# Kernel optimization log

Hardware: AMD Instinct MI355X
Metric: run time of the kernel (lower is better)

Reference implementation:

```python
import jax, jax.numpy as jnp
import numpy as np

H = 128          # hidden/context/decoder dim
HEADS = 4
HEAD_DIM = H // HEADS
MAX_LENGTH = 64
VOCAB = 3


def _lstm_step(h, c, x, Wih, Whh, b):
    # PyTorch gate order: i, f, g, o
    gates = x @ Wih.T + h @ Whh.T + b
    i, f, g, o = jnp.split(gates, 4, axis=-1)
    c = jax.nn.sigmoid(f) * c + jax.nn.sigmoid(i) * jnp.tanh(g)
    h = jax.nn.sigmoid(o) * jnp.tanh(c)
    return h, c


def _run_lstm(x, Wih, Whh, b):
    # x: (T, B, D) -> (T, B, H); zero initial state (PyTorch default)
    B = x.shape[1]
    Hh = Whh.shape[1]
    init = (jnp.zeros((B, Hh), x.dtype), jnp.zeros((B, Hh), x.dtype))
    def step(carry, xt):
        h, c = carry
        h, c = _lstm_step(h, c, xt, Wih, Whh, b)
        return (h, c), h
    _, ys = jax.lax.scan(step, init, x)
    return ys


def setup_inputs() -> dict:
    key = jax.random.key(0)
    T, B, D = 512, 64, 1024
    ks = jax.random.split(key, 20)
    def p(k, shape, s=0.05):
        return jax.random.normal(k, shape, dtype=jnp.float32) * s
    return {
        "cnn_output": p(ks[0], (T, B, D), 1.0),
        # encoder LSTM (2 layers); biases fused (b_ih + b_hh)
        "enc_Wih0": p(ks[1], (4 * H, D)),
        "enc_Whh0": p(ks[2], (4 * H, H)),
        "enc_b0": p(ks[3], (4 * H,)),
        "enc_Wih1": p(ks[4], (4 * H, H)),
        "enc_Whh1": p(ks[5], (4 * H, H)),
        "enc_b1": p(ks[6], (4 * H,)),
        # MultiheadAttention(embed_dim=128, num_heads=4)
        "attn_in_w": p(ks[7], (3 * H, H)),
        "attn_in_b": p(ks[8], (3 * H,)),
        "attn_out_w": p(ks[9], (H, H)),
        "attn_out_b": p(ks[10], (H,)),
        # decoder LSTM (2 layers), input dim 256
        "dec_Wih0": p(ks[11], (4 * H, 2 * H)),
        "dec_Whh0": p(ks[12], (4 * H, H)),
        "dec_b0": p(ks[13], (4 * H,)),
        "dec_Wih1": p(ks[14], (4 * H, H)),
        "dec_Whh1": p(ks[15], (4 * H, H)),
        "dec_b1": p(ks[16], (4 * H,)),
        # output projection
        "lin_w": p(ks[17], (VOCAB, H)),
        "lin_b": p(ks[18], (VOCAB,)),
    }


def reference(cnn_output, enc_Wih0, enc_Whh0, enc_b0, enc_Wih1, enc_Whh1, enc_b1,
              attn_in_w, attn_in_b, attn_out_w, attn_out_b,
              dec_Wih0, dec_Whh0, dec_b0, dec_Wih1, dec_Whh1, dec_b1,
              lin_w, lin_b):
    T, B, _ = cnn_output.shape
    # ---- encoder: 2-layer LSTM over T ----
    enc = _run_lstm(cnn_output, enc_Wih0, enc_Whh0, enc_b0)
    enc = _run_lstm(enc, enc_Wih1, enc_Whh1, enc_b1)          # (T, B, H)

    # ---- precompute attention keys/values (encoding is fixed) ----
    Wq, Wk, Wv = jnp.split(attn_in_w, 3, axis=0)
    bq, bk, bv = jnp.split(attn_in_b, 3, axis=0)
    K = (enc @ Wk.T + bk).reshape(T, B, HEADS, HEAD_DIM)      # (T,B,h,d)
    V = (enc @ Wv.T + bv).reshape(T, B, HEADS, HEAD_DIM)
    scale = 1.0 / np.sqrt(HEAD_DIM)

    # ---- 64-step attention + 2-layer LSTM decode loop ----
    out0 = jnp.zeros((B, H), cnn_output.dtype)
    h0 = jnp.zeros((2, B, H), cnn_output.dtype)
    c0 = jnp.zeros((2, B, H), cnn_output.dtype)

    def step(carry, _):
        out, h, c = carry
        q = ((out @ Wq.T + bq) * scale).reshape(B, HEADS, HEAD_DIM)
        scores = jnp.einsum("bhd,tbhd->bht", q, K)            # (B,h,T)
        attn = jax.nn.softmax(scores, axis=-1)
        ctx = jnp.einsum("bht,tbhd->bhd", attn, V).reshape(B, H)
        ctx = ctx @ attn_out_w.T + attn_out_b
        x = jnp.concatenate([out, ctx], axis=-1)              # (B, 2H)
        nh0, nc0 = _lstm_step(h[0], c[0], x, dec_Wih0, dec_Whh0, dec_b0)
        nh1, nc1 = _lstm_step(h[1], c[1], nh0, dec_Wih1, dec_Whh1, dec_b1)
        new_out = jax.nn.relu(nh1)
        y = new_out @ lin_w.T + lin_b                          # (B, vocab)
        return (new_out, jnp.stack([nh0, nh1]), jnp.stack([nc0, nc1])), y

    _, ys = jax.lax.scan(step, (out0, h0, c0), None, length=MAX_LENGTH)
    return ys                                                  # (64, B, vocab)
```

## Files before the change

kernel.cpp:

```cpp
#include <hip/hip_runtime.h>
#include <math.h>

#define T_LEN 512
#define BATCH 64
#define HID 128
#define G4 512

#define OFF_WQ2   0
#define OFF_WXO   16384
#define OFF_WXC   81920
#define OFF_WHH0b 147456
#define OFF_WIH1b 212992
#define OFF_WHH1b 278528
#define W2_TOTAL  344064

typedef __attribute__((ext_vector_type(8))) short short8b;
typedef __attribute__((ext_vector_type(4))) float f32x4;

__device__ __forceinline__ float sigf(float x) { return 1.0f / (1.0f + __expf(-x)); }
__device__ __forceinline__ float tanhfast(float x) {
    float e = __expf(2.f * x);
    return 1.f - 2.f / (e + 1.f);
}

__device__ __forceinline__ unsigned short f2bf(float x) {
    unsigned u = __float_as_uint(x);
    unsigned r = (u + 0x7fffu + ((u >> 16) & 1u)) >> 16;
    return (unsigned short)r;
}
__device__ __forceinline__ float bf2f(unsigned short u) {
    return __uint_as_float((unsigned)u << 16);
}

__device__ __forceinline__ void cvt8(uint4 u, float f[8]) {
    f[0] = __uint_as_float(u.x << 16); f[1] = __uint_as_float(u.x & 0xffff0000u);
    f[2] = __uint_as_float(u.y << 16); f[3] = __uint_as_float(u.y & 0xffff0000u);
    f[4] = __uint_as_float(u.z << 16); f[5] = __uint_as_float(u.z & 0xffff0000u);
    f[6] = __uint_as_float(u.w << 16); f[7] = __uint_as_float(u.w & 0xffff0000u);
}

#define KEEP4(Vv) asm volatile("" : "+v"((Vv).x), "+v"((Vv).y), "+v"((Vv).z), "+v"((Vv).w))

__device__ __forceinline__ void cstore(float* p, float v) {
    __hip_atomic_store(p, v, __ATOMIC_RELAXED, __HIP_MEMORY_SCOPE_AGENT);
}
__device__ __forceinline__ float cload(float* p) {
    return __hip_atomic_load(p, __ATOMIC_RELAXED, __HIP_MEMORY_SCOPE_AGENT);
}

__global__ __launch_bounds__(256) void pack_bf(
    const float* __restrict__ src, unsigned short* __restrict__ dst, long n8)
{
    long i = (long)blockIdx.x * 256 + threadIdx.x;
    long stride = (long)gridDim.x * 256;
    for (; i < n8; i += stride) {
        const float* s = src + i * 8;
        float4 a = *(const float4*)s;
        float4 b = *(const float4*)(s + 4);
        uint4 o;
        o.x = (unsigned)f2bf(a.x) | ((unsigned)f2bf(a.y) << 16);
        o.y = (unsigned)f2bf(a.z) | ((unsigned)f2bf(a.w) << 16);
        o.z = (unsigned)f2bf(b.x) | ((unsigned)f2bf(b.y) << 16);
        o.w = (unsigned)f2bf(b.z) | ((unsigned)f2bf(b.w) << 16);
        *(uint4*)(dst + i * 8) = o;
    }
}

__global__ __launch_bounds__(256) void gemm_mfma_bf16(
    const unsigned short* __restrict__ A, const unsigned short* __restrict__ B,
    const float* __restrict__ bias, unsigned short* __restrict__ C,
    int M, int N, int K)
{
    __shared__ __align__(16) unsigned char As[128 * 128];
    __shared__ __align__(16) unsigned char Bs[128 * 128];
    const int tid = threadIdx.x;
    const int lane = tid & 63, wave = tid >> 6;
    const int wr = wave >> 1, wc = wave & 1;
    const int m0 = blockIdx.y * 128, n0 = blockIdx.x * 128;
    f32x4 acc[4][4] = {};
    const int lr = lane & 15, g = lane >> 4;

    for (int k0 = 0; k0 < K; k0 += 64) {
        __syncthreads();
        #pragma unroll
        for (int i = 0; i < 4; ++i) {
            int c = tid + i * 256;
            int row = c >> 3, cb = (c & 7) * 16;
            int swz = cb ^ ((row & 7) << 4);
            uint4 va = *(const uint4*)(A + (size_t)(m0 + row) * K + k0 + (c & 7) * 8);
            *(uint4*)(As + row * 128 + swz) = va;
            uint4 vb = *(const uint4*)(B + (size_t)(n0 + row) * K + k0 + (c & 7) * 8);
            *(uint4*)(Bs + row * 128 + swz) = vb;
        }
        __syncthreads();
        #pragma unroll
        for (int kh = 0; kh < 2; ++kh) {
            const int cb = kh * 64 + g * 16;
            short8b af[4], bfr[4];
            #pragma unroll
            for (int m = 0; m < 4; ++m) {
                int row = wr * 64 + m * 16 + lr;
                af[m] = *(const short8b*)(As + row * 128 + (cb ^ ((row & 7) << 4)));
            }
            #pragma unroll
            for (int n = 0; n < 4; ++n) {
                int row = wc * 64 + n * 16 + lr;
                bfr[n] = *(const short8b*)(Bs + row * 128 + (cb ^ ((row & 7) << 4)));
            }
            #pragma unroll
            for (int m = 0; m < 4; ++m)
                #pragma unroll
                for (int n = 0; n < 4; ++n)
                    acc[m][n] = __builtin_amdgcn_mfma_f32_16x16x32_bf16(
                        af[m], bfr[n], acc[m][n], 0, 0, 0);
        }
    }
    #pragma unroll
    for (int n = 0; n < 4; ++n) {
        int col = n0 + wc * 64 + n * 16 + lr;
        float bv = bias[col];
        #pragma unroll
        for (int m = 0; m < 4; ++m) {
            #pragma unroll
            for (int j = 0; j < 4; ++j) {
                int row = m0 + wr * 64 + m * 16 + g * 4 + j;
                C[(size_t)row * N + col] = f2bf(acc[m][n][j] + bv);
            }
        }
    }
}

__global__ __launch_bounds__(1024) void lstm_rec3(
    const unsigned short* __restrict__ X,
    const float* __restrict__ Whh,
    unsigned short* __restrict__ HoutB)
{
    const int b = blockIdx.x;
    const int tid = threadIdx.x;
    const int r = tid >> 1, half = tid & 1;
    __shared__ __align__(16) float h_s[HID];
    __shared__ float gate_s[G4];
    float4 w4[16];
    {
        const float4* wr4 = (const float4*)(Whh + (size_t)r * HID + half * 64);
        #pragma unroll
        for (int i = 0; i < 16; ++i) w4[i] = wr4[i];
    }
    float c = 0.f;
    if (tid < HID) h_s[tid] = 0.f;
    __syncthreads();
    float xc0 = 0.f, xc1 = 0.f, xc2 = 0.f, xc3 = 0.f;
    if (half == 0) {
        xc0 = bf2f(X[(size_t)(0 * BATCH + b) * G4 + r]);
        xc1 = bf2f(X[(size_t)(1 * BATCH + b) * G4 + r]);
        xc2 = bf2f(X[(size_t)(2 * BATCH + b) * G4 + r]);
        xc3 = bf2f(X[(size_t)(3 * BATCH + b) * G4 + r]);
    }
    for (int tc = 0; tc < T_LEN; tc += 4) {
        float xn0 = 0.f, xn1 = 0.f, xn2 = 0.f, xn3 = 0.f;
        if (half == 0 && tc + 4 < T_LEN) {
            xn0 = bf2f(X[(size_t)((tc + 4) * BATCH + b) * G4 + r]);
            xn1 = bf2f(X[(size_t)((tc + 5) * BATCH + b) * G4 + r]);
            xn2 = bf2f(X[(size_t)((tc + 6) * BATCH + b) * G4 + r]);
            xn3 = bf2f(X[(size_t)((tc + 7) * BATCH + b) * G4 + r]);
        }
        #pragma unroll
        for (int i = 0; i < 4; ++i) {
            const int t = tc + i;
            const float xv = (i == 0) ? xc0 : (i == 1) ? xc1 : (i == 2) ? xc2 : xc3;
            float a0 = 0.f, a1 = 0.f, a2 = 0.f, a3 = 0.f;
            const float4* h4 = (const float4*)(h_s + half * 64);
            #pragma unroll
            for (int k = 0; k < 16; ++k) {
                float4 hv = h4[k];
                a0 = fmaf(w4[k].x, hv.x, a0);
                a1 = fmaf(w4[k].y, hv.y, a1);
                a2 = fmaf(w4[k].z, hv.z, a2);
                a3 = fmaf(w4[k].w, hv.w, a3);
            }
            float tot = (a0 + a1) + (a2 + a3);
            tot += __shfl_xor(tot, 1);
            if (half == 0) gate_s[r] = tot + xv;
            __syncthreads();
            if (tid < HID) {
                float gi = gate_s[tid], gf = gate_s[HID+tid], gg = gate_s[2*HID+tid], go = gate_s[3*HID+tid];
                c = sigf(gf) * c + sigf(gi) * tanhfast(gg);
                float h = sigf(go) * tanhfast(c);
                h_s[tid] = h;
                HoutB[(size_t)(t * BATCH + b) * HID + tid] = f2bf(h);
            }
            __syncthreads();
        }
        xc0 = xn0; xc1 = xn1; xc2 = xn2; xc3 = xn3;
    }
}

__global__ __launch_bounds__(256) void kv_pack_bf(
    const unsigned short* __restrict__ KVbf, unsigned short* __restrict__ Kb,
    unsigned short* __restrict__ Vt)
{
    const int b = blockIdx.x & 63, tc = blockIdx.x >> 6;
    const int t0 = tc * 128;
    __shared__ unsigned short tile[128][130];
    const int half = threadIdx.x >> 7;
    const int d = threadIdx.x & 127;
    for (int tt = 0; tt < 128; tt += 2) {
        int trow = tt + half;
        int t = t0 + trow;
        const unsigned short* src = KVbf + ((size_t)t * BATCH + b) * 256;
        Kb[((size_t)b * T_LEN + t) * HID + d] = src[d];
        tile[trow][d] = src[128 + d];
    }
    __syncthreads();
    for (int dd = 0; dd < 128; dd += 2) {
        int drow = dd + half;
        int ts = threadIdx.x & 127;
        Vt[((size_t)b * HID + drow) * T_LEN + t0 + ts] = tile[ts][drow];
    }
}

__global__ __launch_bounds__(256) void pack2(
    const float* __restrict__ attn_in_w,
    const float* __restrict__ dWih0, const float* __restrict__ dWhh0,
    const float* __restrict__ dWih1, const float* __restrict__ dWhh1,
    unsigned short* __restrict__ Wb2)
{
    int i = blockIdx.x * 256 + threadIdx.x;
    if (i >= W2_TOTAL) return;
    if (i >= OFF_WXC && i < OFF_WHH0b) return;
    float v;
    if (i < OFF_WXO) v = attn_in_w[i];
    else if (i < OFF_WXC) {
        int j = i - OFF_WXO; v = dWih0[(size_t)(j >> 7) * 256 + (j & 127)];
    }
    else if (i < OFF_WIH1b) v = dWhh0[i - OFF_WHH0b];
    else if (i < OFF_WHH1b) v = dWih1[i - OFF_WIH1b];
    else                    v = dWhh1[i - OFF_WHH1b];
    Wb2[i] = f2bf(v);
}

__global__ __launch_bounds__(256) void fuse_wxc(
    const float* __restrict__ dWih0, const float* __restrict__ ow,
    unsigned short* __restrict__ Wb2)
{
    __shared__ float ow_s[128 * 128];
    for (int i = threadIdx.x; i < 16384; i += 256) ow_s[i] = ow[i];
    __syncthreads();
    const int r = blockIdx.x * 2 + (threadIdx.x >> 7);
    const int c = threadIdx.x & 127;
    const float* wr = dWih0 + (size_t)r * 256 + 128;
    float acc = 0.f;
    #pragma unroll 8
    for (int j = 0; j < 128; ++j) acc = fmaf(wr[j], ow_s[j * 128 + c], acc);
    Wb2[OFF_WXC + r * 128 + c] = f2bf(acc);
}

__global__ __launch_bounds__(128) void fuse_b0(
    const float* __restrict__ dWih0, const float* __restrict__ ob,
    const float* __restrict__ db0, float* __restrict__ b0p)
{
    int r = blockIdx.x * 128 + threadIdx.x;
    const float* wr = dWih0 + (size_t)r * 256 + 128;
    float acc = db0[r];
    #pragma unroll 8
    for (int j = 0; j < 128; ++j) acc = fmaf(wr[j], ob[j], acc);
    b0p[r] = acc;
}

__global__ __launch_bounds__(512, 2) void decoder7(
    const unsigned short* __restrict__ Kb, const unsigned short* __restrict__ Vt,
    const unsigned short* __restrict__ Wb2, const float* __restrict__ b0p,
    const float* __restrict__ attn_b, const float* __restrict__ b1,
    const float* __restrict__ lw, const float* __restrict__ lb,
    int* __restrict__ flags, float* __restrict__ exh0, float* __restrict__ exh1,
    float* __restrict__ Y)
{
    extern __shared__ __align__(16) char dyn[];
    char* Kl = dyn;
    const int wid = blockIdx.x;
    const int b = wid & 63;
    const int half64 = wid >> 6;
    const int dbase = half64 * 64;
    const int pbase = 64 - dbase;
    const int tid = threadIdx.x;
    int* myflag = flags + wid * 16;
    int* pflag  = flags + (wid ^ 64) * 16;
    float* exh0b = exh0 + b * 256;
    float* exh1b = exh1 + b * 256;

    __shared__ __align__(16) float x_s[384];
    __shared__ __align__(16) float x1_s[256];
    __shared__ __align__(16) float q_s[HID];
    __shared__ __align__(16) float sc[4 * T_LEN];
    __shared__ float red[512];
    __shared__ __align__(16) float ctxp[4][HID];
    __shared__ float g_s[256];
    __shared__ float hmax[4], hden[4];

    {
        const unsigned short* Ksrc = Kb + (size_t)b * T_LEN * HID;
        for (int c = tid; c < T_LEN * HID / 8; c += 512) {
            int t = c >> 4, k16 = c & 15;
            uint4 v = *(const uint4*)(Ksrc + c * 8);
            *(uint4*)(Kl + t * 256 + ((k16 * 16) ^ ((t & 15) << 4))) = v;
        }
    }
    const int lr = tid >> 1, halfk = tid & 1;
    const int r0 = (lr >> 6) * 128 + dbase + (lr & 63);
    uint4 W0[24], W1[16], WQ[4];
    #pragma unroll
    for (int i = 0; i < 24; ++i) {
        int ge = halfk * 192 + i * 8;
        const unsigned short* src =
            (ge < 128) ? Wb2 + OFF_WXO   + (size_t)r0 * HID + ge
          : (ge < 256) ? Wb2 + OFF_WXC   + (size_t)r0 * HID + (ge - 128)
                       : Wb2 + OFF_WHH0b + (size_t)r0 * HID + (ge - 256);
        W0[i] = *(const uint4*)src;
    }
    #pragma unroll
    for (int i = 0; i < 16; ++i) {
        int ge = halfk * 128 + i * 8;
        const unsigned short* src =
            (ge < 128) ? Wb2 + OFF_WIH1b + (size_t)r0 * HID + ge
                       : Wb2 + OFF_WHH1b + (size_t)r0 * HID + (ge - 128);
        W1[i] = *(const uint4*)src;
    }
    const int qrow = tid >> 2, qpart = tid & 3;
    #pragma unroll
    for (int i = 0; i < 4; ++i)
        WQ[i] = *(const uint4*)(Wb2 + OFF_WQ2 + (size_t)qrow * HID + qpart * 32 + i * 8);
    #pragma unroll
    for (int i = 0; i < 24; ++i) KEEP4(W0[i]);
    #pragma unroll
    for (int i = 0; i < 16; ++i) KEEP4(W1[i]);
    #pragma unroll
    for (int i = 0; i < 4; ++i) KEEP4(WQ[i]);

    const float b0r = b0p[r0];
    const float b1r = b1[r0];
    const float bqv = attn_b[qrow];
    float c0 = 0.f, c1 = 0.f;
    if (tid < 384) x_s[tid] = 0.f;
    if (tid < 256) x1_s[tid] = 0.f;
    __syncthreads();
    const float scale = 0.17677669529663687f;
    const int g = tid >> 7, l = tid & 127;

    for (int step = 0; step < 64; ++step) {
        #pragma unroll
        for (int i = 0; i < 24; ++i) KEEP4(W0[i]);
        #pragma unroll
        for (int i = 0; i < 16; ++i) KEEP4(W1[i]);
        #pragma unroll
        for (int i = 0; i < 4; ++i) KEEP4(WQ[i]);
        const int par = step & 1;
        if (step > 0) {
            if (tid == 0)
                while (__hip_atomic_load(pflag, __ATOMIC_RELAXED, __HIP_MEMORY_SCOPE_AGENT) < 2*step + 1)
                    __builtin_amdgcn_s_sleep(1);
            asm volatile("" ::: "memory");
            __syncthreads();
            if (tid < 64) {
                float hp = cload(&exh1b[((step - 1) & 1) * 128 + pbase + tid]);
                x1_s[128 + pbase + tid] = hp;
                x_s[pbase + tid] = fmaxf(hp, 0.f);
            }
            __syncthreads();
        }
        if (step > 0 && half64 == 0 && tid < 24) {
            const int row = tid >> 3, part = tid & 7;
            const float* wr = lw + row * HID + part * 16;
            const float* os = x_s + part * 16;
            float acc = 0.f;
            #pragma unroll
            for (int k = 0; k < 16; ++k) acc = fmaf(wr[k], os[k], acc);
            acc += __shfl_xor(acc, 1);
            acc += __shfl_xor(acc, 2);
            acc += __shfl_xor(acc, 4);
            if (part == 0) Y[((size_t)(step - 1) * BATCH + b) * 3 + row] = acc + lb[row];
        }
        {
            float acc = 0.f;
            const float* os = x_s + qpart * 32;
            #pragma unroll
            for (int i = 0; i < 4; ++i) {
                float f[8]; cvt8(WQ[i], f);
                const float* o8 = os + i * 8;
                acc += f[0]*o8[0]+f[1]*o8[1]+f[2]*o8[2]+f[3]*o8[3]
                     + f[4]*o8[4]+f[5]*o8[5]+f[6]*o8[6]+f[7]*o8[7];
            }
            acc += __shfl_xor(acc, 1);
            acc += __shfl_xor(acc, 2);
            if (qpart == 0) q_s[qrow] = (acc + bqv) * scale;
        }
        __syncthreads();
        {
            const int t = tid;
            float acc[4] = {0.f, 0.f, 0.f, 0.f};
            #pragma unroll
            for (int k16 = 0; k16 < 16; ++k16) {
                uint4 u = *(const uint4*)(Kl + t * 256 + ((k16 * 16) ^ ((t & 15) << 4)));
                float f[8]; cvt8(u, f);
                float4 q0 = *(const float4*)(q_s + k16 * 8);
                float4 q1 = *(const float4*)(q_s + k16 * 8 + 4);
                acc[k16 >> 2] += f[0]*q0.x + f[1]*q0.y + f[2]*q0.z + f[3]*q0.w
                               + f[4]*q1.x + f[5]*q1.y + f[6]*q1.z + f[7]*q1.w;
            }
            #pragma unroll
            for (int h = 0; h < 4; ++h) sc[h * T_LEN + t] = acc[h];
        }
        __syncthreads();
        float v[4];
        float mx = -3.4e38f;
        #pragma unroll
        for (int i = 0; i < 4; ++i) { v[i] = sc[g*T_LEN + l + 128*i]; mx = fmaxf(mx, v[i]); }
        red[tid] = mx;
        __syncthreads();
        if (l < 64) {
            float m2 = fmaxf(red[g*128 + l], red[g*128 + l + 64]);
            #pragma unroll
            for (int s = 32; s > 0; s >>= 1) m2 = fmaxf(m2, __shfl_xor(m2, s, 64));
            if (l == 0) hmax[g] = m2;
        }
        __syncthreads();
        float hm = hmax[g];
        float s4 = 0.f;
        #pragma unroll
        for (int i = 0; i < 4; ++i) {
            float e = __expf(v[i] - hm);
            sc[g*T_LEN + l + 128*i] = e;
            s4 += e;
        }
        red[tid] = s4;
        __syncthreads();
        if (l < 64) {
            float s2 = red[g*128 + l] + red[g*128 + l + 64];
            #pragma unroll
            for (int s = 32; s > 0; s >>= 1) s2 += __shfl_xor(s2, s, 64);
            if (l == 0) hden[g] = s2;
        }
        __syncthreads();
        {
            const int d = tid & 127, ch = tid >> 7;
            const unsigned short* vr = Vt + ((size_t)b * HID + d) * T_LEN + ch * 128;
            const float* scr = sc + (d >> 5) * T_LEN + ch * 128;
            float acc = 0.f;
            #pragma unroll
            for (int k = 0; k < 128; k += 8) {
                float f[8]; cvt8(*(const uint4*)(vr + k), f);
                #pragma unroll
                for (int j = 0; j < 8; ++j) acc = fmaf(f[j], scr[k + j], acc);
            }
            ctxp[ch][d] = acc;
        }
        __syncthreads();
        if (tid < HID)
            x_s[HID + tid] = (ctxp[0][tid] + ctxp[1][tid] + ctxp[2][tid] + ctxp[3][tid]) / hden[tid >> 5];
        __syncthreads();
        {
            float acc = 0.f;
            #pragma unroll
            for (int i = 0; i < 24; ++i) {
                float f[8]; cvt8(W0[i], f);
                const float* xp = x_s + halfk * 192 + i * 8;
                acc += f[0]*xp[0]+f[1]*xp[1]+f[2]*xp[2]+f[3]*xp[3]
                     + f[4]*xp[4]+f[5]*xp[5]+f[6]*xp[6]+f[7]*xp[7];
            }
            acc += __shfl_xor(acc, 1);
            if (halfk == 0) g_s[lr] = acc + b0r;
        }
        __syncthreads();
        if (tid < 64) {
            float gi = g_s[tid], gf = g_s[64+tid], gg = g_s[128+tid], go = g_s[192+tid];
            c0 = sigf(gf) * c0 + sigf(gi) * tanhf(gg);
            float h = sigf(go) * tanhf(c0);
            x_s[256 + dbase + tid] = h;
            x1_s[dbase + tid] = h;
            cstore(&exh0b[par * 128 + dbase + tid], h);
        }
        __syncthreads();
        if (tid == 0) {
            asm volatile("s_waitcnt vmcnt(0)" ::: "memory");
            __hip_atomic_store(myflag, 2*step + 2, __ATOMIC_RELEASE, __HIP_MEMORY_SCOPE_AGENT);
        }
        if (tid == 0)
            while (__hip_atomic_load(pflag, __ATOMIC_ACQUIRE, __HIP_MEMORY_SCOPE_AGENT) < 2*step + 2)
                __builtin_amdgcn_s_sleep(1);
        asm volatile("" ::: "memory");
        __syncthreads();
        if (tid < 64) {
            float hp = cload(&exh0b[par * 128 + pbase + tid]);
            x_s[256 + pbase + tid] = hp;
            x1_s[pbase + tid] = hp;
        }
        __syncthreads();
        {
            float acc = 0.f;
            #pragma unroll
            for (int i = 0; i < 16; ++i) {
                float f[8]; cvt8(W1[i], f);
                const float* xp = x1_s + halfk * 128 + i * 8;
                acc += f[0]*xp[0]+f[1]*xp[1]+f[2]*xp[2]+f[3]*xp[3]
                     + f[4]*xp[4]+f[5]*xp[5]+f[6]*xp[6]+f[7]*xp[7];
            }
            acc += __shfl_xor(acc, 1);
            if (halfk == 0) g_s[lr] = acc + b1r;
        }
        __syncthreads();
        if (tid < 64) {
            float gi = g_s[tid], gf = g_s[64+tid], gg = g_s[128+tid], go = g_s[192+tid];
            c1 = sigf(gf) * c1 + sigf(gi) * tanhf(gg);
            float h = sigf(go) * tanhf(c1);
            x1_s[128 + dbase + tid] = h;
            x_s[dbase + tid] = fmaxf(h, 0.f);
            cstore(&exh1b[par * 128 + dbase + tid], h);
        }
        __syncthreads();
        if (tid == 0) {
            asm volatile("s_waitcnt vmcnt(0)" ::: "memory");
            __hip_atomic_store(myflag, 2*step + 3, __ATOMIC_RELEASE, __HIP_MEMORY_SCOPE_AGENT);
        }
        __syncthreads();
    }
    if (tid == 0)
        while (__hip_atomic_load(pflag, __ATOMIC_ACQUIRE, __HIP_MEMORY_SCOPE_AGENT) < 129)
            __builtin_amdgcn_s_sleep(1);
    asm volatile("" ::: "memory");
    __syncthreads();
    if (tid < 64)
        x_s[pbase + tid] = fmaxf(cload(&exh1b[128 + pbase + tid]), 0.f);
    __syncthreads();
    if (half64 == 0 && tid < 24) {
        const int row = tid >> 3, part = tid & 7;
        const float* wr = lw + row * HID + part * 16;
        const float* os = x_s + part * 16;
        float acc = 0.f;
        #pragma unroll
        for (int k = 0; k < 16; ++k) acc = fmaf(wr[k], os[k], acc);
        acc += __shfl_xor(acc, 1);
        acc += __shfl_xor(acc, 2);
        acc += __shfl_xor(acc, 4);
        if (part == 0) Y[((size_t)63 * BATCH + b) * 3 + row] = acc + lb[row];
    }
}

extern "C" void kernel_launch(void* const* d_in, const int* in_sizes, int n_in,
                              void* d_out, int out_size, void* d_ws, size_t ws_size,
                              hipStream_t stream) {
    const float* cnn        = (const float*)d_in[0];
    const float* eWih0      = (const float*)d_in[1];
    const float* eWhh0      = (const float*)d_in[2];
    const float* eb0        = (const float*)d_in[3];
    const float* eWih1      = (const float*)d_in[4];
    const float* eWhh1      = (const float*)d_in[5];
    const float* eb1        = (const float*)d_in[6];
    const float* attn_in_w  = (const float*)d_in[7];
    const float* attn_in_b  = (const float*)d_in[8];
    const float* attn_out_w = (const float*)d_in[9];
    const float* attn_out_b = (const float*)d_in[10];
    const float* dWih0      = (const float*)d_in[11];
    const float* dWhh0      = (const float*)d_in[12];
    const float* db0        = (const float*)d_in[13];
    const float* dWih1      = (const float*)d_in[14];
    const float* dWhh1      = (const float*)d_in[15];
    const float* db1        = (const float*)d_in[16];
    const float* lin_w      = (const float*)d_in[17];
    const float* lin_b      = (const float*)d_in[18];
    float* Y  = (float*)d_out;

    const int M = T_LEN * BATCH;

    char* wsb = (char*)d_ws;
    unsigned short* Xbf   = (unsigned short*)(wsb);
    unsigned short* Hbf   = (unsigned short*)(wsb + ((size_t)32 << 20));
    unsigned short* wih0b = (unsigned short*)(wsb + ((size_t)40 << 20));
    unsigned short* wih1b = (unsigned short*)(wsb + ((size_t)41 << 20));
    unsigned short* wkvb  = (unsigned short*)(wsb + ((size_t)41 << 20) + (512 << 10));
    unsigned short* Wb2   = (unsigned short*)(wsb + ((size_t)42 << 20));
    float* b0p   = (float*)(wsb + ((size_t)43 << 20));
    int*   flags = (int*)((char*)b0p + 4096);
    float* exh0  = (float*)((char*)flags + 16384);
    float* exh1  = exh0 + 64 * 256;
    unsigned short* cnn_bf = (unsigned short*)(wsb + ((size_t)44 << 20));
    unsigned short* KVbf   = cnn_bf;
    unsigned short* Kb     = (unsigned short*)(wsb + ((size_t)60 << 20));
    unsigned short* Vt     = (unsigned short*)(wsb + ((size_t)68 << 20));

    (void)hipFuncSetAttribute((const void*)decoder7,
                              hipFuncAttributeMaxDynamicSharedMemorySize, 131072);

    pack_bf<<<2048, 256, 0, stream>>>(cnn, cnn_bf, (long)M * 1024 / 8);
    pack_bf<<<256, 256, 0, stream>>>(eWih0, wih0b, (long)512 * 1024 / 8);
    pack_bf<<<32, 256, 0, stream>>>(eWih1, wih1b, (long)512 * 128 / 8);
    pack_bf<<<16, 256, 0, stream>>>(attn_in_w + 128 * 128, wkvb, (long)256 * 128 / 8);
    gemm_mfma_bf16<<<dim3(4, M/128), 256, 0, stream>>>(cnn_bf, wih0b, eb0, Xbf, M, 512, 1024);
    (void)hipMemsetAsync(flags, 0, 16384 + 2 * 64 * 256 * 4, stream);
    pack2<<<(W2_TOTAL + 255) / 256, 256, 0, stream>>>(attn_in_w, dWih0, dWhh0, dWih1, dWhh1, Wb2);
    fuse_wxc<<<256, 256, 0, stream>>>(dWih0, attn_out_w, Wb2);
    fuse_b0<<<4, 128, 0, stream>>>(dWih0, attn_out_b, db0, b0p);
    lstm_rec3<<<BATCH, 1024, 0, stream>>>(Xbf, eWhh0, Hbf);
    gemm_mfma_bf16<<<dim3(4, M/128), 256, 0, stream>>>(Hbf, wih1b, eb1, Xbf, M, 512, 128);
    lstm_rec3<<<BATCH, 1024, 0, stream>>>(Xbf, eWhh1, Hbf);
    gemm_mfma_bf16<<<dim3(2, M/128), 256, 0, stream>>>(Hbf, wkvb, attn_in_b + 128, KVbf, M, 256, 128);
    kv_pack_bf<<<256, 256, 0, stream>>>(KVbf, Kb, Vt);
    decoder7<<<128, 512, 131072, stream>>>(Kb, Vt, Wb2, b0p,
                                           attn_in_b, db1, lin_w, lin_b,
                                           flags, exh0, exh1, Y);
}
```

Before: 2.468 ms.

## Shuffle-exchange LSTM gates, double-buffer hidden state, drop softmax max pass

The encoder LSTM recurrence remaps threads so that the four gate rows of one hidden unit sit in the same wavefront. Gates are exchanged with lane shuffles instead of shared memory, and the hidden state is double-buffered, which removes one block barrier per timestep. The decoder drops the softmax max-subtraction pass, exponentiating raw scores directly, and reduces the context partial sums with shuffles instead of a shared-memory round trip. Skipping the max subtraction removes two barriers and a reduction, but it risks overflow if attention scores grow large.

```diff
diff --git a/kernel.cpp b/kernel.cpp
--- a/kernel.cpp
+++ b/kernel.cpp
@@ -130,16 +130,20 @@
     }
 }
 
-__global__ __launch_bounds__(1024) void lstm_rec3(
+__global__ __launch_bounds__(1024) void lstm_rec4(
     const unsigned short* __restrict__ X,
     const float* __restrict__ Whh,
     unsigned short* __restrict__ HoutB)
 {
     const int b = blockIdx.x;
     const int tid = threadIdx.x;
-    const int r = tid >> 1, half = tid & 1;
-    __shared__ __align__(16) float h_s[HID];
-    __shared__ float gate_s[G4];
+    const int j = tid >> 3;
+    const int gg = (tid >> 1) & 3;
+    const int half = tid & 1;
+    const int r = gg * 128 + j;
+    const int lane = tid & 63;
+    const int base = lane & ~7;
+    __shared__ __align__(16) float h_s[2][HID];
     float4 w4[16];
     {
         const float4* wr4 = (const float4*)(Whh + (size_t)r * HID + half * 64);
@@ -147,7 +151,7 @@
         for (int i = 0; i < 16; ++i) w4[i] = wr4[i];
     }
     float c = 0.f;
-    if (tid < HID) h_s[tid] = 0.f;
+    if (tid < HID) h_s[0][tid] = 0.f;
     __syncthreads();
     float xc0 = 0.f, xc1 = 0.f, xc2 = 0.f, xc3 = 0.f;
     if (half == 0) {
@@ -167,9 +171,10 @@
         #pragma unroll
         for (int i = 0; i < 4; ++i) {
             const int t = tc + i;
+            const int rb = t & 1, wb = rb ^ 1;
             const float xv = (i == 0) ? xc0 : (i == 1) ? xc1 : (i == 2) ? xc2 : xc3;
             float a0 = 0.f, a1 = 0.f, a2 = 0.f, a3 = 0.f;
-            const float4* h4 = (const float4*)(h_s + half * 64);
+            const float4* h4 = (const float4*)(&h_s[rb][0] + half * 64);
             #pragma unroll
             for (int k = 0; k < 16; ++k) {
                 float4 hv = h4[k];
@@ -180,14 +185,16 @@
             }
             float tot = (a0 + a1) + (a2 + a3);
             tot += __shfl_xor(tot, 1);
-            if (half == 0) gate_s[r] = tot + xv;
-            __syncthreads();
-            if (tid < HID) {
-                float gi = gate_s[tid], gf = gate_s[HID+tid], gg = gate_s[2*HID+tid], go = gate_s[3*HID+tid];
-                c = sigf(gf) * c + sigf(gi) * tanhfast(gg);
-                float h = sigf(go) * tanhfast(c);
-                h_s[tid] = h;
-                HoutB[(size_t)(t * BATCH + b) * HID + tid] = f2bf(h);
+            float gv = tot + xv;
+            float gi_ = __shfl(gv, base + 0, 64);
+            float gf_ = __shfl(gv, base + 2, 64);
+            float gc_ = __shfl(gv, base + 4, 64);
+            float go_ = __shfl(gv, base + 6, 64);
+            c = sigf(gf_) * c + sigf(gi_) * tanhfast(gc_);
+            float h = sigf(go_) * tanhfast(c);
+            if ((tid & 7) == 0) {
+                h_s[wb][j] = h;
+                HoutB[(size_t)(t * BATCH + b) * HID + j] = f2bf(h);
             }
             __syncthreads();
         }
@@ -267,7 +274,7 @@
     b0p[r] = acc;
 }
 
-__global__ __launch_bounds__(512, 2) void decoder7(
+__global__ __launch_bounds__(512, 2) void decoder7b(
     const unsigned short* __restrict__ Kb, const unsigned short* __restrict__ Vt,
     const unsigned short* __restrict__ Wb2, const float* __restrict__ b0p,
     const float* __restrict__ attn_b, const float* __restrict__ b1,
@@ -293,9 +300,8 @@
     __shared__ __align__(16) float q_s[HID];
     __shared__ __align__(16) float sc[4 * T_LEN];
     __shared__ float red[512];
-    __shared__ __align__(16) float ctxp[4][HID];
     __shared__ float g_s[256];
-    __shared__ float hmax[4], hden[4];
+    __shared__ float hden[4];
 
     {
         const unsigned short* Ksrc = Kb + (size_t)b * T_LEN * HID;
@@ -407,31 +413,15 @@
                                + f[4]*q1.x + f[5]*q1.y + f[6]*q1.z + f[7]*q1.w;
             }
             #pragma unroll
-            for (int h = 0; h < 4; ++h) sc[h * T_LEN + t] = acc[h];
-        }
-        __syncthreads();
-        float v[4];
-        float mx = -3.4e38f;
-        #pragma unroll
-        for (int i = 0; i < 4; ++i) { v[i] = sc[g*T_LEN + l + 128*i]; mx = fmaxf(mx, v[i]); }
-        red[tid] = mx;
-        __syncthreads();
-        if (l < 64) {
-            float m2 = fmaxf(red[g*128 + l], red[g*128 + l + 64]);
-            #pragma unroll
-            for (int s = 32; s > 0; s >>= 1) m2 = fmaxf(m2, __shfl_xor(m2, s, 64));
-            if (l == 0) hmax[g] = m2;
-        }
-        __syncthreads();
-        float hm = hmax[g];
-        float s4 = 0.f;
-        #pragma unroll
-        for (int i = 0; i < 4; ++i) {
-            float e = __expf(v[i] - hm);
-            sc[g*T_LEN + l + 128*i] = e;
-            s4 += e;
-        }
-        red[tid] = s4;
+            for (int h = 0; h < 4; ++h) sc[h * T_LEN + t] = __expf(acc[h]);
+        }
+        __syncthreads();
+        {
+            float s4 = 0.f;
+            #pragma unroll
+            for (int i = 0; i < 4; ++i) s4 += sc[g * T_LEN + l + 128 * i];
+            red[tid] = s4;
+        }
         __syncthreads();
         if (l < 64) {
             float s2 = red[g*128 + l] + red[g*128 + l + 64];
@@ -441,7 +431,7 @@
         }
         __syncthreads();
         {
-            const int d = tid & 127, ch = tid >> 7;
+            const int d = tid >> 2, ch = tid & 3;
             const unsigned short* vr = Vt + ((size_t)b * HID + d) * T_LEN + ch * 128;
             const float* scr = sc + (d >> 5) * T_LEN + ch * 128;
             float acc = 0.f;
@@ -451,11 +441,10 @@
                 #pragma unroll
                 for (int j = 0; j < 8; ++j) acc = fmaf(f[j], scr[k + j], acc);
             }
-            ctxp[ch][d] = acc;
-        }
-        __syncthreads();
-        if (tid < HID)
-            x_s[HID + tid] = (ctxp[0][tid] + ctxp[1][tid] + ctxp[2][tid] + ctxp[3][tid]) / hden[tid >> 5];
+            acc += __shfl_xor(acc, 1);
+            acc += __shfl_xor(acc, 2);
+            if (ch == 0) x_s[HID + d] = acc / hden[d >> 5];
+        }
         __syncthreads();
         {
             float acc = 0.f;
@@ -586,7 +575,7 @@
     unsigned short* Kb     = (unsigned short*)(wsb + ((size_t)60 << 20));
     unsigned short* Vt     = (unsigned short*)(wsb + ((size_t)68 << 20));
 
-    (void)hipFuncSetAttribute((const void*)decoder7,
+    (void)hipFuncSetAttribute((const void*)decoder7b,
                               hipFuncAttributeMaxDynamicSharedMemorySize, 131072);
 
     pack_bf<<<2048, 256, 0, stream>>>(cnn, cnn_bf, (long)M * 1024 / 8);
@@ -598,12 +587,12 @@
     pack2<<<(W2_TOTAL + 255) / 256, 256, 0, stream>>>(attn_in_w, dWih0, dWhh0, dWih1, dWhh1, Wb2);
     fuse_wxc<<<256, 256, 0, stream>>>(dWih0, attn_out_w, Wb2);
     fuse_b0<<<4, 128, 0, stream>>>(dWih0, attn_out_b, db0, b0p);
-    lstm_rec3<<<BATCH, 1024, 0, stream>>>(Xbf, eWhh0, Hbf);
+    lstm_rec4<<<BATCH, 1024, 0, stream>>>(Xbf, eWhh0, Hbf);
     gemm_mfma_bf16<<<dim3(4, M/128), 256, 0, stream>>>(Hbf, wih1b, eb1, Xbf, M, 512, 128);
-    lstm_rec3<<<BATCH, 1024, 0, stream>>>(Xbf, eWhh1, Hbf);
+    lstm_rec4<<<BATCH, 1024, 0, stream>>>(Xbf, eWhh1, Hbf);
     gemm_mfma_bf16<<<dim3(2, M/128), 256, 0, stream>>>(Hbf, wkvb, attn_in_b + 128, KVbf, M, 256, 128);
     kv_pack_bf<<<256, 256, 0, stream>>>(KVbf, Kb, Vt);
-    decoder7<<<128, 512, 131072, stream>>>(Kb, Vt, Wb2, b0p,
-                                           attn_in_b, db1, lin_w, lin_b,
-                                           flags, exh0, exh1, Y);
-}
+    decoder7b<<<128, 512, 131072, stream>>>(Kb, Vt, Wb2, b0p,
+                                            attn_in_b, db1, lin_w, lin_b,
+                                            flags, exh0, exh1, Y);
+}
```

New measurement: 2.615 ms. +5.9%, slower.
